# Kernel optimization log

Measured on AMD Instinct MI355X. Metric: run time of the kernel, lower is better.

Reference implementation:

```python
import jax, jax.numpy as jnp
import numpy as np

BN_EPS = 1e-5

def _conv1x1(x, w, b):
    # x: [B,C,H,W], w: [O,C], b: [O] -> [B,O,H,W]
    return jnp.einsum('bchw,oc->bohw', x, w) + b[None, :, None, None]

def _maxpool2(x):
    B, C, H, W = x.shape
    return x.reshape(B, C, H // 2, 2, W // 2, 2).max(axis=(3, 5))

def setup_inputs() -> dict:
    key = jax.random.key(0)
    ks = jax.random.split(key, 5)
    B, C, Cint, H, W = 8, 512, 256, 64, 64
    s = 1.0 / np.sqrt(C)
    s2 = 1.0 / np.sqrt(Cint)
    return {
        'x': jax.random.normal(ks[0], (B, C, H, W), jnp.float32),
        'g_w': jax.random.normal(ks[1], (Cint, C), jnp.float32) * s,
        'g_b': jnp.zeros((Cint,), jnp.float32),
        'theta_w': jax.random.normal(ks[2], (Cint, C), jnp.float32) * s,
        'theta_b': jnp.zeros((Cint,), jnp.float32),
        'phi_w': jax.random.normal(ks[3], (Cint, C), jnp.float32) * s,
        'phi_b': jnp.zeros((Cint,), jnp.float32),
        'w_w': jax.random.normal(ks[4], (C, Cint), jnp.float32) * s2,
        'w_b': jnp.zeros((C,), jnp.float32),
        'bn_gamma': jnp.ones((C,), jnp.float32),
        'bn_beta': jnp.zeros((C,), jnp.float32),
        'bn_mean': jnp.zeros((C,), jnp.float32),
        'bn_var': jnp.ones((C,), jnp.float32),
    }

def reference(x, g_w, g_b, theta_w, theta_b, phi_w, phi_b, w_w, w_b,
              bn_gamma, bn_beta, bn_mean, bn_var):
    B, C, H, W = x.shape
    Cint = g_w.shape[0]
    # projections (1x1 convs); g and phi are sub-sampled by MaxPool2d(2)
    xg = _maxpool2(_conv1x1(x, g_w, g_b)).reshape(B, Cint, -1)      # [B,Cint,M]
    xphi = _maxpool2(_conv1x1(x, phi_w, phi_b)).reshape(B, Cint, -1)  # [B,Cint,M]
    xth = _conv1x1(x, theta_w, theta_b).reshape(B, Cint, -1)        # [B,Cint,N]
    # affinity: theta^T @ phi -> [B,N,M], softmax over M
    f = jax.nn.softmax(jnp.einsum('bcn,bcm->bnm', xth, xphi), axis=-1)
    # weighted sum: f @ g^T -> [B,N,Cint] -> [B,Cint,H,W]
    y = jnp.einsum('bnm,bcm->bcn', f, xg).reshape(B, Cint, H, W)
    # output conv + batchnorm (inference form) + residual
    z = _conv1x1(y, w_w, w_b)
    inv = jax.lax.rsqrt(bn_var + BN_EPS)
    z = (z - bn_mean[None, :, None, None]) * (bn_gamma * inv)[None, :, None, None] + bn_beta[None, :, None, None]
    return z + x
```

## Files before the change

### kernel.cpp

```cpp
#include <hip/hip_runtime.h>
#include <cmath>


#define B_  8
#define C_  512
#define CI_ 256
#define N_  4096
#define M_  1024

typedef _Float16 half8 __attribute__((ext_vector_type(8)));
typedef _Float16 half4 __attribute__((ext_vector_type(4)));
typedef float    f32x4 __attribute__((ext_vector_type(4)));

static __device__ __forceinline__ unsigned pkh(float a, float b) {
    _Float16 ha = (_Float16)a, hb = (_Float16)b;
    unsigned short ua = __builtin_bit_cast(unsigned short, ha);
    unsigned short ub = __builtin_bit_cast(unsigned short, hb);
    return (unsigned)ua | ((unsigned)ub << 16);
}

__global__ __launch_bounds__(256) void wconv_kernel(
    const float* __restrict__ g_w, const float* __restrict__ th_w,
    const float* __restrict__ ph_w, const float* __restrict__ w_w,
    _Float16* __restrict__ wAll, _Float16* __restrict__ w16)
{
    const int i = blockIdx.x * 256 + threadIdx.x;
    if (i < 768 * 512) {
        const int o = i >> 9, c = i & 511;
        const float v = (o < 256) ? g_w[o * 512 + c]
                      : (o < 512) ? th_w[(o - 256) * 512 + c]
                                  : ph_w[(o - 512) * 512 + c];
        wAll[i] = (_Float16)v;
    } else {
        const int j = i - 768 * 512;
        w16[j] = (_Float16)w_w[j];
    }
}

__global__ __launch_bounds__(256) void xt_kernel(
    const float* __restrict__ x, _Float16* __restrict__ xT)
{
    __shared__ float Ls[64][68];
    const int t = threadIdx.x;
    const int n0 = blockIdx.x * 64, c0 = blockIdx.y * 64, b = blockIdx.z;

    const int row = t >> 4, coln = (t & 15) * 4;
    #pragma unroll
    for (int p = 0; p < 4; ++p) {
        const int c = p * 16 + row;
        *(float4*)&Ls[c][coln] = *(const float4*)&x[((size_t)b * C_ + c0 + c) * N_ + n0 + coln];
    }
    __syncthreads();
    const int nr = t >> 2, cq = (t & 3) * 16;
    _Float16 hv[16];
    #pragma unroll
    for (int j = 0; j < 16; ++j) hv[j] = (_Float16)Ls[cq + j][nr];
    _Float16* dst = &xT[((size_t)b * N_ + n0 + nr) * C_ + c0 + cq];
    *(half8*)&dst[0] = *(half8*)&hv[0];
    *(half8*)&dst[8] = *(half8*)&hv[8];
}

__global__ __launch_bounds__(256) void proj_kernel(
    const _Float16* __restrict__ xT, const _Float16* __restrict__ wAll,
    const float* __restrict__ g_b, const float* __restrict__ th_b,
    const float* __restrict__ ph_b,
    _Float16* __restrict__ thT, _Float16* __restrict__ phT, _Float16* __restrict__ g16)
{
    __shared__ __align__(16) char smem[27648];
    _Float16 (*Ws)[72] = (_Float16(*)[72])smem;
    _Float16 (*Xs)[72] = (_Float16(*)[72])(smem + 9216);
    _Float16 (*Yt)[72] = (_Float16(*)[72])smem;
    _Float16 (*Pp)[72] = (_Float16(*)[72])smem;
    _Float16 (*Pg)[40] = (_Float16(*)[40])smem;

    const int t = threadIdx.x;
    const int w = t >> 6, l = t & 63, l15 = l & 15, lg = l >> 4;
    const int bx = blockIdx.x, rt = blockIdx.y, b = blockIdx.z;
    const int r0 = rt * 64, n0 = bx * 128;

    f32x4 acc[8];
    #pragma unroll
    for (int f = 0; f < 8; ++f) acc[f] = (f32x4){0.f, 0.f, 0.f, 0.f};

    const int warow = t >> 2, wakq = (t & 3) * 16;
    const int xrow = t >> 1,  xkq = (t & 1) * 32;

    #pragma unroll 1
    for (int k0 = 0; k0 < C_; k0 += 64) {
        __syncthreads();
        {
            const _Float16* src = &wAll[(size_t)(r0 + warow) * C_ + k0 + wakq];
            *(half8*)&Ws[warow][wakq]     = *(const half8*)&src[0];
            *(half8*)&Ws[warow][wakq + 8] = *(const half8*)&src[8];
            const _Float16* xs = &xT[((size_t)b * N_ + n0 + xrow) * C_ + k0 + xkq];
            *(half8*)&Xs[xrow][xkq]      = *(const half8*)&xs[0];
            *(half8*)&Xs[xrow][xkq + 8]  = *(const half8*)&xs[8];
            *(half8*)&Xs[xrow][xkq + 16] = *(const half8*)&xs[16];
            *(half8*)&Xs[xrow][xkq + 24] = *(const half8*)&xs[24];
        }
        __syncthreads();
        #pragma unroll
        for (int ks = 0; ks < 2; ++ks) {
            half8 a = *(half8*)&Ws[w * 16 + l15][ks * 32 + lg * 8];
            #pragma unroll
            for (int f = 0; f < 8; ++f) {
                half8 bb = *(half8*)&Xs[f * 16 + l15][ks * 32 + lg * 8];
                acc[f] = __builtin_amdgcn_mfma_f32_16x16x32_f16(a, bb, acc[f], 0, 0, 0);
            }
        }
    }

    {
        const float* Bp = (rt < 4) ? g_b : (rt < 8) ? th_b : ph_b;
        const int coff = (rt < 4) ? 0 : (rt < 8) ? 256 : 512;
        float bias[4];
        #pragma unroll
        for (int r = 0; r < 4; ++r) bias[r] = Bp[r0 - coff + w * 16 + lg * 4 + r];
        #pragma unroll
        for (int f = 0; f < 8; ++f)
            #pragma unroll
            for (int r = 0; r < 4; ++r) acc[f][r] += bias[r];
    }

    if (rt >= 4 && rt < 8) {
        const int c0 = r0 - 256;
        __syncthreads();
        #pragma unroll
        for (int f = 0; f < 8; ++f) {
            half4 hv = { (_Float16)acc[f][0], (_Float16)acc[f][1],
                         (_Float16)acc[f][2], (_Float16)acc[f][3] };
            *(half4*)&Yt[f * 16 + l15][w * 16 + lg * 4] = hv;
        }
        __syncthreads();
        const int nr = t >> 1, oq = (t & 1) * 32;
        _Float16* dst = &thT[((size_t)b * N_ + n0 + nr) * CI_ + c0 + oq];
        #pragma unroll
        for (int j = 0; j < 4; ++j)
            *(half8*)&dst[j * 8] = *(half8*)&Yt[nr][oq + j * 8];
    } else {
        float pool[4][4];
        #pragma unroll
        for (int f = 0; f < 4; ++f)
            #pragma unroll
            for (int r = 0; r < 4; ++r) {
                const float v0 = acc[f][r], v1 = acc[f + 4][r];
                const float h0 = fmaxf(v0, __shfl_xor(v0, 1));
                const float h1 = fmaxf(v1, __shfl_xor(v1, 1));
                pool[f][r] = fmaxf(h0, h1);
            }
        __syncthreads();
        const bool isphi = (rt >= 8);
        const int c0 = isphi ? r0 - 512 : r0;
        if ((l15 & 1) == 0) {
            const int Wl = l15 >> 1;
            if (isphi) {
                #pragma unroll
                for (int f = 0; f < 4; ++f) {
                    half4 hv = { (_Float16)pool[f][0], (_Float16)pool[f][1],
                                 (_Float16)pool[f][2], (_Float16)pool[f][3] };
                    *(half4*)&Pp[f * 8 + Wl][w * 16 + lg * 4] = hv;
                }
            } else {
                #pragma unroll
                for (int f = 0; f < 4; ++f)
                    #pragma unroll
                    for (int r = 0; r < 4; ++r)
                        Pg[w * 16 + lg * 4 + r][f * 8 + Wl] = (_Float16)pool[f][r];
            }
        }
        __syncthreads();
        if (isphi) {
            const int row = t >> 3, cqq = (t & 7) * 8;
            *(half8*)&phT[((size_t)b * M_ + bx * 32 + row) * CI_ + c0 + cqq] =
                *(half8*)&Pp[row][cqq];
        } else {
            const int row = t >> 2, mq = (t & 3) * 8;
            *(half8*)&g16[((size_t)b * CI_ + r0 + row) * M_ + bx * 32 + mq] =
                *(half8*)&Pg[row][mq];
        }
    }
}

__global__ __launch_bounds__(256, 3) void attn_kernel(
    const _Float16* __restrict__ thT, const _Float16* __restrict__ phT,
    const _Float16* __restrict__ g16, _Float16* __restrict__ y16)
{
    __shared__ __align__(16) char smem[52224];
    _Float16 (*Ph)[264] = (_Float16(*)[264])smem;
    _Float16 (*Gl)[72]  = (_Float16(*)[72])(smem + 33792);

    const int t = threadIdx.x;
    const int w = t >> 6, l = t & 63;
    const int l15 = l & 15, lg = l >> 4;
    const int n0 = blockIdx.x * 64;
    const int b  = blockIdx.y;
    const int n  = n0 + w * 16 + l15;

    half8 ta[8];
    {
        const _Float16* src = &thT[((size_t)b * N_ + n) * CI_ + lg * 8];
        #pragma unroll
        for (int kc = 0; kc < 8; ++kc)
            ta[kc] = *(const half8*)&src[kc * 32];
    }

    f32x4 yacc[16];
    #pragma unroll
    for (int i = 0; i < 16; ++i) yacc[i] = (f32x4){0.f, 0.f, 0.f, 0.f};
    float m_run = -INFINITY, l_run = 0.f;

    const int phrow = t >> 2, phseg = (t & 3) * 64;
    const int glrow = t >> 1, glseg = (t & 1) * 32;

    const int baseA = ((lg & 1) * 2) * 16 + l15;
    const int baseB = baseA + 16;
    const bool hi = ((lg >> 1) & 1) != 0;

    #pragma unroll 1
    for (int mt = 0; mt < 16; ++mt) {
        const int m0 = mt * 64;

        __syncthreads();
        {
            const _Float16* src = &phT[((size_t)b * M_ + m0 + phrow) * CI_ + phseg];
            #pragma unroll
            for (int j = 0; j < 8; ++j)
                *(half8*)&Ph[phrow][phseg + j * 8] = *(const half8*)&src[j * 8];
        }
        __syncthreads();

        f32x4 sf[4];
        #pragma unroll
        for (int i = 0; i < 4; ++i) sf[i] = (f32x4){0.f, 0.f, 0.f, 0.f};
        #pragma unroll
        for (int kc = 0; kc < 8; ++kc) {
            #pragma unroll
            for (int mf = 0; mf < 4; ++mf) {
                half8 a = *(half8*)&Ph[mf * 16 + l15][kc * 32 + lg * 8];
                sf[mf] = __builtin_amdgcn_mfma_f32_16x16x32_f16(a, ta[kc], sf[mf], 0, 0, 0);
            }
        }

        float mx = sf[0][0];
        #pragma unroll
        for (int mf = 0; mf < 4; ++mf)
            #pragma unroll
            for (int r = 0; r < 4; ++r) mx = fmaxf(mx, sf[mf][r]);
        mx = fmaxf(mx, __shfl_xor(mx, 16, 64));
        mx = fmaxf(mx, __shfl_xor(mx, 32, 64));
        const float mnew = fmaxf(m_run, mx);
        const float scl = __expf(m_run - mnew);
        float s = 0.f;
        unsigned u0[4], u1[4];
        #pragma unroll
        for (int mf = 0; mf < 4; ++mf) {
            const float p0 = __expf(sf[mf][0] - mnew);
            const float p1 = __expf(sf[mf][1] - mnew);
            const float p2 = __expf(sf[mf][2] - mnew);
            const float p3 = __expf(sf[mf][3] - mnew);
            s += (p0 + p1) + (p2 + p3);
            u0[mf] = pkh(p0, p1);
            u1[mf] = pkh(p2, p3);
        }
        s += __shfl_xor(s, 16, 64);
        s += __shfl_xor(s, 32, 64);
        l_run = l_run * scl + s;
        m_run = mnew;
        #pragma unroll
        for (int i = 0; i < 16; ++i) {
            yacc[i][0] *= scl; yacc[i][1] *= scl;
            yacc[i][2] *= scl; yacc[i][3] *= scl;
        }

        half8 pb[2];
        #pragma unroll
        for (int ks = 0; ks < 2; ++ks) {
            const unsigned a0 = __shfl(u0[2 * ks],     baseA, 64);
            const unsigned a1 = __shfl(u1[2 * ks],     baseA, 64);
            const unsigned c0 = __shfl(u0[2 * ks + 1], baseA, 64);
            const unsigned c1 = __shfl(u1[2 * ks + 1], baseA, 64);
            const unsigned b0 = __shfl(u0[2 * ks],     baseB, 64);
            const unsigned b1 = __shfl(u1[2 * ks],     baseB, 64);
            const unsigned d0 = __shfl(u0[2 * ks + 1], baseB, 64);
            const unsigned d1 = __shfl(u1[2 * ks + 1], baseB, 64);
            union { unsigned u[4]; half8 h; } cv;
            cv.u[0] = hi ? c0 : a0;
            cv.u[1] = hi ? c1 : a1;
            cv.u[2] = hi ? d0 : b0;
            cv.u[3] = hi ? d1 : b1;
            pb[ks] = cv.h;
        }

        #pragma unroll
        for (int ch = 0; ch < 2; ++ch) {
            __syncthreads();
            {
                const _Float16* src = &g16[((size_t)b * CI_ + ch * 128 + glrow) * M_ + m0 + glseg];
                #pragma unroll
                for (int j = 0; j < 4; ++j)
                    *(half8*)&Gl[glrow][glseg + j * 8] = *(const half8*)&src[j * 8];
            }
            __syncthreads();
            #pragma unroll
            for (int cf = 0; cf < 8; ++cf) {
                half8 a0 = *(half8*)&Gl[cf * 16 + l15][lg * 8];
                half8 a1 = *(half8*)&Gl[cf * 16 + l15][32 + lg * 8];
                yacc[ch * 8 + cf] = __builtin_amdgcn_mfma_f32_16x16x32_f16(a0, pb[0], yacc[ch * 8 + cf], 0, 0, 0);
                yacc[ch * 8 + cf] = __builtin_amdgcn_mfma_f32_16x16x32_f16(a1, pb[1], yacc[ch * 8 + cf], 0, 0, 0);
            }
        }
    }

    const float linv = 1.f / l_run;
    _Float16* dst = &y16[((size_t)b * N_ + n) * CI_];
    #pragma unroll
    for (int q = 0; q < 16; ++q) {
        half4 hv = { (_Float16)(yacc[q][0] * linv), (_Float16)(yacc[q][1] * linv),
                     (_Float16)(yacc[q][2] * linv), (_Float16)(yacc[q][3] * linv) };
        *(half4*)&dst[q * 16 + lg * 4] = hv;
    }
}

__global__ __launch_bounds__(256) void out_kernel(
    const _Float16* __restrict__ y16, const _Float16* __restrict__ w16,
    const float* __restrict__ w_b,
    const float* __restrict__ bn_g, const float* __restrict__ bn_b,
    const float* __restrict__ bn_m, const float* __restrict__ bn_v,
    const float* __restrict__ x, float* __restrict__ out)
{
    __shared__ __align__(16) char smem[33792];
    _Float16 (*Ws)[72] = (_Float16(*)[72])smem;
    _Float16 (*Ys)[72] = (_Float16(*)[72])(smem + 9216);
    float    (*Yt)[132] = (float(*)[132])smem;

    const int t = threadIdx.x;
    const int w = t >> 6, l = t & 63, l15 = l & 15, lg = l >> 4;
    const int bx = blockIdx.x, by = blockIdx.y, b = blockIdx.z;
    const int r0 = by * 64, n0 = bx * 128;

    f32x4 acc[8];
    #pragma unroll
    for (int f = 0; f < 8; ++f) acc[f] = (f32x4){0.f, 0.f, 0.f, 0.f};

    const int warow = t >> 2, wakq = (t & 3) * 16;
    const int yrow = t >> 1,  ykq = (t & 1) * 32;

    #pragma unroll 1
    for (int k0 = 0; k0 < CI_; k0 += 64) {
        __syncthreads();
        {
            const _Float16* src = &w16[(size_t)(r0 + warow) * CI_ + k0 + wakq];
            *(half8*)&Ws[warow][wakq]     = *(const half8*)&src[0];
            *(half8*)&Ws[warow][wakq + 8] = *(const half8*)&src[8];
            const _Float16* ys = &y16[((size_t)b * N_ + n0 + yrow) * CI_ + k0 + ykq];
            *(half8*)&Ys[yrow][ykq]      = *(const half8*)&ys[0];
            *(half8*)&Ys[yrow][ykq + 8]  = *(const half8*)&ys[8];
            *(half8*)&Ys[yrow][ykq + 16] = *(const half8*)&ys[16];
            *(half8*)&Ys[yrow][ykq + 24] = *(const half8*)&ys[24];
        }
        __syncthreads();
        #pragma unroll
        for (int ks = 0; ks < 2; ++ks) {
            half8 a = *(half8*)&Ws[w * 16 + l15][ks * 32 + lg * 8];
            #pragma unroll
            for (int f = 0; f < 8; ++f) {
                half8 bb = *(half8*)&Ys[f * 16 + l15][ks * 32 + lg * 8];
                acc[f] = __builtin_amdgcn_mfma_f32_16x16x32_f16(a, bb, acc[f], 0, 0, 0);
            }
        }
    }

    float scp[4], shp[4];
    #pragma unroll
    for (int r = 0; r < 4; ++r) {
        const int c = r0 + w * 16 + lg * 4 + r;
        const float s = bn_g[c] * rsqrtf(bn_v[c] + 1e-5f);
        scp[r] = s;
        shp[r] = bn_b[c] + (w_b[c] - bn_m[c]) * s;
    }
    __syncthreads();
    #pragma unroll
    for (int f = 0; f < 8; ++f)
        #pragma unroll
        for (int r = 0; r < 4; ++r)
            Yt[w * 16 + lg * 4 + r][f * 16 + l15] = acc[f][r] * scp[r] + shp[r];
    __syncthreads();

    const int prow = t >> 5, nq = (t & 31) * 4;
    #pragma unroll
    for (int p = 0; p < 8; ++p) {
        const int row = p * 8 + prow;
        const size_t base = ((size_t)b * C_ + r0 + row) * N_ + n0 + nq;
        const float4 xr = *(const float4*)&x[base];
        float4 v = *(float4*)&Yt[row][nq];
        v.x += xr.x; v.y += xr.y; v.z += xr.z; v.w += xr.w;
        *(float4*)&out[base] = v;
    }
}

extern "C" void kernel_launch(void* const* d_in, const int* in_sizes, int n_in,
                              void* d_out, int out_size, void* d_ws, size_t ws_size,
                              hipStream_t stream) {
    const float* x    = (const float*)d_in[0];
    const float* g_w  = (const float*)d_in[1];
    const float* g_b  = (const float*)d_in[2];
    const float* th_w = (const float*)d_in[3];
    const float* th_b = (const float*)d_in[4];
    const float* ph_w = (const float*)d_in[5];
    const float* ph_b = (const float*)d_in[6];
    const float* w_w  = (const float*)d_in[7];
    const float* w_b  = (const float*)d_in[8];
    const float* bn_g = (const float*)d_in[9];
    const float* bn_b = (const float*)d_in[10];
    const float* bn_m = (const float*)d_in[11];
    const float* bn_v = (const float*)d_in[12];
    float* out = (float*)d_out;

    _Float16* xT   = (_Float16*)d_ws;
    _Float16* wAll = xT + (size_t)B_ * N_ * C_;
    _Float16* w16  = wAll + 768 * 512;
    _Float16* thT  = w16 + 512 * 256;
    _Float16* phT  = thT + (size_t)B_ * N_ * CI_;
    _Float16* g16  = phT + (size_t)B_ * M_ * CI_;
    _Float16* y16  = g16 + (size_t)B_ * M_ * CI_;

    wconv_kernel<<<2048, 256, 0, stream>>>(g_w, th_w, ph_w, w_w, wAll, w16);
    xt_kernel<<<dim3(64, 8, 8), 256, 0, stream>>>(x, xT);
    proj_kernel<<<dim3(32, 12, 8), 256, 0, stream>>>(xT, wAll, g_b, th_b, ph_b,
                                                     thT, phT, g16);
    attn_kernel<<<dim3(64, 8), 256, 0, stream>>>(thT, phT, g16, y16);
    out_kernel<<<dim3(32, 8, 8), 256, 0, stream>>>(y16, w16, w_b, bn_g, bn_b, bn_m, bn_v,
                                                   x, out);
}
```

Before: 348.4 us.

## Load phi and g operands directly from global memory instead of LDS staging

Removes shared-memory staging of the phi and g tiles in the attention kernel; each wave now loads its MFMA operands straight from global memory. This eliminates four block barriers per key tile and the LDS write/read round-trip. In exchange, the four waves of a block redundantly fetch the same data through the cache hierarchy, and the long-latency global loads sit directly in the MFMA chain. The min-blocks occupancy hint is also dropped.

```diff
diff --git a/kernel.cpp b/kernel.cpp
--- a/kernel.cpp
+++ b/kernel.cpp
@@ -181,14 +181,10 @@
     }
 }
 
-__global__ __launch_bounds__(256, 3) void attn_kernel(
+__global__ __launch_bounds__(256) void attn_kernel(
     const _Float16* __restrict__ thT, const _Float16* __restrict__ phT,
     const _Float16* __restrict__ g16, _Float16* __restrict__ y16)
 {
-    __shared__ __align__(16) char smem[52224];
-    _Float16 (*Ph)[264] = (_Float16(*)[264])smem;
-    _Float16 (*Gl)[72]  = (_Float16(*)[72])(smem + 33792);
-
     const int t = threadIdx.x;
     const int w = t >> 6, l = t & 63;
     const int l15 = l & 15, lg = l >> 4;
@@ -204,13 +200,13 @@
             ta[kc] = *(const half8*)&src[kc * 32];
     }
 
+    const _Float16* phbase = &phT[((size_t)b * M_ + l15) * CI_ + lg * 8];
+    const _Float16* gbase  = &g16[((size_t)b * CI_ + l15) * M_ + lg * 8];
+
     f32x4 yacc[16];
     #pragma unroll
     for (int i = 0; i < 16; ++i) yacc[i] = (f32x4){0.f, 0.f, 0.f, 0.f};
     float m_run = -INFINITY, l_run = 0.f;
-
-    const int phrow = t >> 2, phseg = (t & 3) * 64;
-    const int glrow = t >> 1, glseg = (t & 1) * 32;
 
     const int baseA = ((lg & 1) * 2) * 16 + l15;
     const int baseB = baseA + 16;
@@ -219,15 +215,7 @@
     #pragma unroll 1
     for (int mt = 0; mt < 16; ++mt) {
         const int m0 = mt * 64;
-
-        __syncthreads();
-        {
-            const _Float16* src = &phT[((size_t)b * M_ + m0 + phrow) * CI_ + phseg];
-            #pragma unroll
-            for (int j = 0; j < 8; ++j)
-                *(half8*)&Ph[phrow][phseg + j * 8] = *(const half8*)&src[j * 8];
-        }
-        __syncthreads();
+        const _Float16* phm = phbase + (size_t)m0 * CI_;
 
         f32x4 sf[4];
         #pragma unroll
@@ -236,7 +224,7 @@
         for (int kc = 0; kc < 8; ++kc) {
             #pragma unroll
             for (int mf = 0; mf < 4; ++mf) {
-                half8 a = *(half8*)&Ph[mf * 16 + l15][kc * 32 + lg * 8];
+                half8 a = *(const half8*)&phm[(size_t)(mf * 16) * CI_ + kc * 32];
                 sf[mf] = __builtin_amdgcn_mfma_f32_16x16x32_f16(a, ta[kc], sf[mf], 0, 0, 0);
             }
         }
@@ -293,18 +281,11 @@
 
         #pragma unroll
         for (int ch = 0; ch < 2; ++ch) {
-            __syncthreads();
-            {
-                const _Float16* src = &g16[((size_t)b * CI_ + ch * 128 + glrow) * M_ + m0 + glseg];
-                #pragma unroll
-                for (int j = 0; j < 4; ++j)
-                    *(half8*)&Gl[glrow][glseg + j * 8] = *(const half8*)&src[j * 8];
-            }
-            __syncthreads();
             #pragma unroll
             for (int cf = 0; cf < 8; ++cf) {
-                half8 a0 = *(half8*)&Gl[cf * 16 + l15][lg * 8];
-                half8 a1 = *(half8*)&Gl[cf * 16 + l15][32 + lg * 8];
+                const _Float16* gp = gbase + (size_t)(ch * 128 + cf * 16) * M_ + m0;
+                half8 a0 = *(const half8*)&gp[0];
+                half8 a1 = *(const half8*)&gp[32];
                 yacc[ch * 8 + cf] = __builtin_amdgcn_mfma_f32_16x16x32_f16(a0, pb[0], yacc[ch * 8 + cf], 0, 0, 0);
                 yacc[ch * 8 + cf] = __builtin_amdgcn_mfma_f32_16x16x32_f16(a1, pb[1], yacc[ch * 8 + cf], 0, 0, 0);
             }
```

Result: slower. 457.0 us (+31.2%).
